# Optimization experiments

Measured on AMD Instinct MI355X. Metric: run time of the kernel, lower is better.

Reference implementation:

```python
import jax, jax.numpy as jnp
import numpy as np

S = 1
R = 64
INV_T = 100.0
EVAL_STEPS = 7  # module in eval mode
EPS = 1e-6


def setup_inputs() -> dict:
    key = jax.random.key(0)
    kx, kb = jax.random.split(key)
    B, C, H, W = 8, 512, 64, 64
    x = jax.random.uniform(kx, (B, C, H, W), dtype=jnp.float32)  # non-negative input for NMF
    bases = jax.random.uniform(kb, (B * S, C // S, R), dtype=jnp.float32)
    # F.normalize(bases, dim=1): L2-normalize along D
    bases = bases / jnp.linalg.norm(bases, axis=1, keepdims=True)
    return {"x": x, "bases": bases}


def reference(x, bases):
    B, C, H, W = x.shape
    D = C // S
    N = H * W
    xf = x.reshape(B * S, D, N)  # (BS, D, N)

    # initial coefficients: softmax(inv_t * x^T @ bases)
    coef = jax.nn.softmax(INV_T * jnp.einsum('bdn,bdr->bnr', xf, bases), axis=-1)

    def mu_step(carry, _):
        bases, coef = carry
        # update coef: coef *= (x^T bases) / (coef (bases^T bases) + eps)
        num = jnp.einsum('bdn,bdr->bnr', xf, bases)            # (BS, N, R)
        gram_b = jnp.einsum('bdr,bds->brs', bases, bases)      # (BS, R, R)
        coef = coef * num / (jnp.einsum('bnr,brs->bns', coef, gram_b) + EPS)
        # update bases: bases *= (x coef) / (bases (coef^T coef) + eps)
        num_b = jnp.einsum('bdn,bnr->bdr', xf, coef)           # (BS, D, R)
        gram_c = jnp.einsum('bnr,bns->brs', coef, coef)        # (BS, R, R)
        bases = bases * num_b / (jnp.einsum('bdr,brs->bds', bases, gram_c) + EPS)
        return (bases, coef), None

    (bases, coef), _ = jax.lax.scan(mu_step, (bases, coef), None, length=EVAL_STEPS)

    # compute_coef: one extra coef multiplicative update
    num = jnp.einsum('bdn,bdr->bnr', xf, bases)
    gram_b = jnp.einsum('bdr,bds->brs', bases, bases)
    coef = coef * num / (jnp.einsum('bnr,brs->bns', coef, gram_b) + EPS)

    out = jnp.einsum('bdr,bnr->bdn', bases, coef)  # bases @ coef^T
    return out.reshape(B, C, H, W)
```

## Files before the change

kernel.cpp:

```cpp
#include <hip/hip_runtime.h>
#include <math.h>

#define BATCH 8
#define DD 512
#define NN 4096
#define RR 64
#define NSTEPS 7
#define INV_T 100.0f
#define EPSV 1e-6f
#define GC_SCALE (1.0f / 1024.0f)
#define GC_UNSCALE 1024.0f

typedef __attribute__((ext_vector_type(8))) _Float16 f16x8;
typedef __attribute__((ext_vector_type(4))) _Float16 f16x4;
typedef __attribute__((ext_vector_type(4))) float f32x4;

__device__ __forceinline__ _Float16 f2h(float f) { return (_Float16)f; }

__device__ __forceinline__ void do_xcvt(const float* x, _Float16* x_h,
                                        _Float16* xT_h, int b, int d0, int n0,
                                        int tid, char* smem) {
  _Float16(*t)[72] = (_Float16(*)[72])smem;
  const size_t xbase = (size_t)(b * DD + d0) * NN + n0;
#pragma unroll
  for (int i = 0; i < 4; ++i) {
    const int idx = tid + i * 256;
    const int row = idx >> 4, c4 = (idx & 15) * 4;
    const float4 v = *(const float4*)(x + xbase + (size_t)row * NN + c4);
    f16x4 hv = {f2h(v.x), f2h(v.y), f2h(v.z), f2h(v.w)};
    *(f16x4*)(x_h + xbase + (size_t)row * NN + c4) = hv;
    *(f16x4*)&t[row][c4] = hv;
  }
  __syncthreads();
  const size_t tbase = (size_t)(b * NN + n0) * DD + d0;
#pragma unroll
  for (int i = 0; i < 4; ++i) {
    const int idx = tid + i * 256;
    const int row = idx >> 4, c4 = (idx & 15) * 4;
    f16x4 wv = {t[c4][row], t[c4 + 1][row], t[c4 + 2][row], t[c4 + 3][row]};
    *(f16x4*)(xT_h + tbase + (size_t)row * DD + c4) = wv;
  }
}

__device__ __forceinline__ void do_bases_prep(const float* bin, float* bases32,
                                              _Float16* bases_h,
                                              _Float16* basesT_h, int b, int d0,
                                              int tid, char* smem) {
  float(*t)[65] = (float(*)[65])smem;
  const size_t base = (size_t)(b * DD + d0) * RR;
#pragma unroll
  for (int i = 0; i < 4; ++i) {
    const int idx = tid + i * 256;
    const int row = idx >> 4, c4 = (idx & 15) * 4;
    const float4 v = *(const float4*)(bin + base + row * RR + c4);
    *(float4*)(bases32 + base + row * RR + c4) = v;
    f16x4 hv = {f2h(v.x), f2h(v.y), f2h(v.z), f2h(v.w)};
    *(f16x4*)(bases_h + base + row * RR + c4) = hv;
    t[row][c4] = v.x; t[row][c4 + 1] = v.y; t[row][c4 + 2] = v.z; t[row][c4 + 3] = v.w;
  }
  __syncthreads();
#pragma unroll
  for (int i = 0; i < 4; ++i) {
    const int idx = tid + i * 256;
    const int row = idx >> 4, c4 = (idx & 15) * 4;
    f16x4 wv = {f2h(t[c4][row]), f2h(t[c4 + 1][row]), f2h(t[c4 + 2][row]),
                f2h(t[c4 + 3][row])};
    *(f16x4*)(basesT_h + (size_t)(b * RR + row) * DD + d0 + c4) = wv;
  }
}

__device__ __forceinline__ void do_gramb_init(const _Float16* basesT_h,
                                              float* pgb, int b, int tid, int w,
                                              int lo, int hi) {
  const _Float16* ap = basesT_h + (size_t)(b * RR + w * 16 + lo) * DD + hi * 8;
  const _Float16* bp = basesT_h + (size_t)(b * RR + lo) * DD + hi * 8;
  f32x4 acc[4] = {};
#pragma unroll
  for (int ks = 0; ks < 16; ++ks) {
    f16x8 a = *(const f16x8*)(ap + ks * 32);
#pragma unroll
    for (int c = 0; c < 4; ++c) {
      f16x8 bb = *(const f16x8*)(bp + (size_t)c * 16 * DD + ks * 32);
      acc[c] = __builtin_amdgcn_mfma_f32_16x16x32_f16(a, bb, acc[c], 0, 0, 0);
    }
  }
  float* op = pgb + (size_t)(b * 8) * 4096;
#pragma unroll
  for (int c = 0; c < 4; ++c)
#pragma unroll
    for (int r = 0; r < 4; ++r)
      op[(w * 16 + hi * 4 + r) * RR + c * 16 + lo] = acc[c][r];
  for (int sp = 1; sp < 8; ++sp)
    for (int idx = tid; idx < 4096; idx += 256)
      pgb[(size_t)(b * 8 + sp) * 4096 + idx] = 0.f;
}

template <int MODE>
__device__ __forceinline__ void do_coef(const _Float16* xT_h,
                                        const _Float16* basesT_h,
                                        const float* pgb, _Float16* coefT_h,
                                        int b, int nt, int tid, int w, int lo,
                                        int hi, char* smem) {
  _Float16* gsm = (_Float16*)smem;
  _Float16(*ct)[72] = (_Float16(*)[72])(smem + 8192);
  const int n0 = nt * 64;
  if (MODE == 1) {
    for (int idx = tid; idx < 4096; idx += 256) {
      float s = 0.f;
#pragma unroll
      for (int sp = 0; sp < 8; ++sp)
        s += pgb[(size_t)(b * 8 + sp) * 4096 + idx];
      gsm[idx] = f2h(s);
    }
#pragma unroll
    for (int i = 0; i < 2; ++i) {
      const int idx = tid + i * 256;
      const int r = idx >> 3, n8 = (idx & 7) * 8;
      f16x8 vv = *(const f16x8*)(coefT_h + (size_t)(b * RR + r) * NN + n0 + n8);
#pragma unroll
      for (int j = 0; j < 8; ++j) ct[n8 + j][r] = vv[j];
    }
    __syncthreads();
  }

  const _Float16* ap = xT_h + (size_t)(b * NN + n0 + w * 16 + lo) * DD + hi * 8;
  const _Float16* bp = basesT_h + (size_t)(b * RR + lo) * DD + hi * 8;
  f32x4 acc[4] = {};
#pragma unroll
  for (int ks = 0; ks < 16; ++ks) {
    f16x8 a = *(const f16x8*)(ap + ks * 32);
#pragma unroll
    for (int c = 0; c < 4; ++c) {
      f16x8 bb = *(const f16x8*)(bp + (size_t)c * 16 * DD + ks * 32);
      acc[c] = __builtin_amdgcn_mfma_f32_16x16x32_f16(a, bb, acc[c], 0, 0, 0);
    }
  }

  float v[4][4];

  if (MODE == 0) {
#pragma unroll
    for (int reg = 0; reg < 4; ++reg) {
      float m = fmaxf(fmaxf(acc[0][reg], acc[1][reg]),
                      fmaxf(acc[2][reg], acc[3][reg]));
      m = fmaxf(m, __shfl_xor(m, 1));
      m = fmaxf(m, __shfl_xor(m, 2));
      m = fmaxf(m, __shfl_xor(m, 4));
      m = fmaxf(m, __shfl_xor(m, 8));
      float s = 0.f, e[4];
#pragma unroll
      for (int c = 0; c < 4; ++c) {
        e[c] = expf(INV_T * (acc[c][reg] - m));
        s += e[c];
      }
      s += __shfl_xor(s, 1);
      s += __shfl_xor(s, 2);
      s += __shfl_xor(s, 4);
      s += __shfl_xor(s, 8);
      const float inv = 1.f / s;
#pragma unroll
      for (int c = 0; c < 4; ++c) v[c][reg] = e[c] * inv;
    }
  } else {
    f32x4 den[4] = {};
#pragma unroll
    for (int kk = 0; kk < 2; ++kk) {
      f16x8 a = *(const f16x8*)&ct[w * 16 + lo][kk * 32 + hi * 8];
#pragma unroll
      for (int c = 0; c < 4; ++c) {
        f16x8 gv = *(const f16x8*)(gsm + (c * 16 + lo) * RR + kk * 32 + hi * 8);
        den[c] = __builtin_amdgcn_mfma_f32_16x16x32_f16(a, gv, den[c], 0, 0, 0);
      }
    }
#pragma unroll
    for (int reg = 0; reg < 4; ++reg)
#pragma unroll
      for (int c = 0; c < 4; ++c) {
        const float oldc = (float)ct[w * 16 + hi * 4 + reg][c * 16 + lo];
        v[c][reg] = oldc * acc[c][reg] / (den[c][reg] + EPSV);
      }
  }

#pragma unroll
  for (int c = 0; c < 4; ++c) {
    f16x4 t4 = {f2h(v[c][0]), f2h(v[c][1]), f2h(v[c][2]), f2h(v[c][3])};
    *(f16x4*)(coefT_h + (size_t)(b * RR + c * 16 + lo) * NN + n0 + w * 16 + hi * 4) = t4;
  }
}

__device__ __forceinline__ void do_numb(const _Float16* x_h,
                                        const _Float16* coefT_h, float* pnb,
                                        int kc, int dt, int b, int w, int lo,
                                        int hi) {
  const _Float16* ap =
      x_h + (size_t)(b * DD + dt * 64 + w * 16 + lo) * NN + kc * 1024 + hi * 8;
  const _Float16* bp = coefT_h + (size_t)(b * RR + lo) * NN + kc * 1024 + hi * 8;
  f32x4 acc[4] = {};
#pragma unroll 4
  for (int ks = 0; ks < 32; ++ks) {
    f16x8 a = *(const f16x8*)(ap + ks * 32);
#pragma unroll
    for (int c = 0; c < 4; ++c) {
      f16x8 bb = *(const f16x8*)(bp + (size_t)c * 16 * NN + ks * 32);
      acc[c] = __builtin_amdgcn_mfma_f32_16x16x32_f16(a, bb, acc[c], 0, 0, 0);
    }
  }
  float* op = pnb + ((size_t)((b * 4 + kc) * DD) + dt * 64 + w * 16 + hi * 4) * RR;
#pragma unroll
  for (int c = 0; c < 4; ++c)
#pragma unroll
    for (int r = 0; r < 4; ++r) op[r * RR + c * 16 + lo] = acc[c][r];
}

__device__ __forceinline__ void do_gramc(const _Float16* coefT_h, float* pgram,
                                         int sp, int b, int w, int lo, int hi) {
  const int k0 = sp * 256;
  const _Float16* ap = coefT_h + (size_t)(b * RR + w * 16 + lo) * NN + k0 + hi * 8;
  const _Float16* bp = coefT_h + (size_t)(b * RR + lo) * NN + k0 + hi * 8;
  f32x4 acc[4] = {};
#pragma unroll
  for (int ks = 0; ks < 8; ++ks) {
    f16x8 a = *(const f16x8*)(ap + ks * 32);
#pragma unroll
    for (int c = 0; c < 4; ++c) {
      f16x8 bb = *(const f16x8*)(bp + (size_t)c * 16 * NN + ks * 32);
      acc[c] = __builtin_amdgcn_mfma_f32_16x16x32_f16(a, bb, acc[c], 0, 0, 0);
    }
  }
  float* op = pgram + ((size_t)(b * 16 + sp) * RR + w * 16 + hi * 4) * RR;
#pragma unroll
  for (int c = 0; c < 4; ++c)
#pragma unroll
    for (int r = 0; r < 4; ++r) op[r * RR + c * 16 + lo] = acc[c][r];
}

__device__ __forceinline__ void do_bases_upd(const float* pnb,
                                             const float* pgram, float* bases32,
                                             _Float16* bases_h,
                                             _Float16* basesT_h, float* pgb,
                                             int dt, int b, int tid, int tx,
                                             int ty, char* smem) {
  float* bsm = (float*)smem;
  _Float16* gsh = (_Float16*)(smem + 16640);
  float* bg = bases32 + (size_t)(b * DD + dt * 64) * RR;
  for (int idx = tid; idx < 4096; idx += 256) {
    const int row = idx >> 6, cc = idx & 63;
    bsm[row * 65 + cc] = bg[row * 64 + cc];
  }
  for (int idx = tid; idx < 4096; idx += 256) {
    float s = 0.f;
#pragma unroll
    for (int sp = 0; sp < 16; ++sp)
      s += pgram[(size_t)(b * 16 + sp) * 4096 + idx];
    gsh[idx] = f2h(s * GC_SCALE);
  }
  __syncthreads();

  float nb[4][4];
#pragma unroll
  for (int i = 0; i < 4; ++i) {
    float4 s = make_float4(0.f, 0.f, 0.f, 0.f);
#pragma unroll
    for (int kc = 0; kc < 4; ++kc) {
      const float4 vv = *(const float4*)(pnb +
          (((size_t)b * 4 + kc) * DD + dt * 64 + ty * 4 + i) * RR + tx * 4);
      s.x += vv.x; s.y += vv.y; s.z += vv.z; s.w += vv.w;
    }
    nb[i][0] = s.x; nb[i][1] = s.y; nb[i][2] = s.z; nb[i][3] = s.w;
  }

  float den[4][4] = {};
  for (int s = 0; s < 64; ++s) {
    float a[4];
#pragma unroll
    for (int i = 0; i < 4; ++i) a[i] = bsm[(ty * 4 + i) * 65 + s];
    const f16x4 gv = *(const f16x4*)&gsh[s * 64 + tx * 4];
    const float g4[4] = {(float)gv[0], (float)gv[1], (float)gv[2], (float)gv[3]};
#pragma unroll
    for (int i = 0; i < 4; ++i)
#pragma unroll
      for (int j = 0; j < 4; ++j) den[i][j] = fmaf(a[i], g4[j], den[i][j]);
  }

  float v[4][4];
#pragma unroll
  for (int i = 0; i < 4; ++i) {
    float4 vv;
#pragma unroll
    for (int j = 0; j < 4; ++j) {
      const float oldb = bsm[(ty * 4 + i) * 65 + tx * 4 + j];
      v[i][j] = oldb * nb[i][j] / fmaf(den[i][j], GC_UNSCALE, EPSV);
    }
    vv.x = v[i][0]; vv.y = v[i][1]; vv.z = v[i][2]; vv.w = v[i][3];
    *(float4*)&bg[(ty * 4 + i) * 64 + tx * 4] = vv;
    f16x4 bv = {f2h(v[i][0]), f2h(v[i][1]), f2h(v[i][2]), f2h(v[i][3])};
    *(f16x4*)(bases_h + (size_t)(b * DD + dt * 64 + ty * 4 + i) * RR + tx * 4) = bv;
  }
#pragma unroll
  for (int j = 0; j < 4; ++j) {
    f16x4 tv = {f2h(v[0][j]), f2h(v[1][j]), f2h(v[2][j]), f2h(v[3][j])};
    *(f16x4*)(basesT_h + (size_t)(b * RR + tx * 4 + j) * DD + dt * 64 + ty * 4) = tv;
  }
  __syncthreads();
#pragma unroll
  for (int i = 0; i < 4; ++i)
#pragma unroll
    for (int j = 0; j < 4; ++j) bsm[(ty * 4 + i) * 65 + tx * 4 + j] = v[i][j];
  __syncthreads();

  float pa[4][4] = {};
  for (int d = 0; d < 64; ++d) {
    float a[4], bb[4];
#pragma unroll
    for (int i = 0; i < 4; ++i) a[i] = bsm[d * 65 + ty * 4 + i];
#pragma unroll
    for (int j = 0; j < 4; ++j) bb[j] = bsm[d * 65 + tx * 4 + j];
#pragma unroll
    for (int i = 0; i < 4; ++i)
#pragma unroll
      for (int j = 0; j < 4; ++j) pa[i][j] = fmaf(a[i], bb[j], pa[i][j]);
  }
  float* pp = pgb + (size_t)(b * 8 + dt) * 4096;
#pragma unroll
  for (int i = 0; i < 4; ++i) {
    float4 vv = make_float4(pa[i][0], pa[i][1], pa[i][2], pa[i][3]);
    *(float4*)(pp + (ty * 4 + i) * 64 + tx * 4) = vv;
  }
}

__device__ __forceinline__ void do_out(const _Float16* bases_h,
                                       const _Float16* coefT_h, float* out,
                                       int nt, int dt, int b, int tid, int w,
                                       int lo, int hi, char* smem) {
  _Float16(*ct)[72] = (_Float16(*)[72])smem;
  const int n0 = nt * 64;
#pragma unroll
  for (int i = 0; i < 2; ++i) {
    const int idx = tid + i * 256;
    const int r = idx >> 3, n8 = (idx & 7) * 8;
    f16x8 vv = *(const f16x8*)(coefT_h + (size_t)(b * RR + r) * NN + n0 + n8);
#pragma unroll
    for (int j = 0; j < 8; ++j) ct[n8 + j][r] = vv[j];
  }
  __syncthreads();
  const _Float16* ap =
      bases_h + (size_t)(b * DD + dt * 64 + w * 16 + lo) * RR + hi * 8;
  f32x4 acc[4] = {};
#pragma unroll
  for (int kk = 0; kk < 2; ++kk) {
    f16x8 a = *(const f16x8*)(ap + kk * 32);
#pragma unroll
    for (int c = 0; c < 4; ++c) {
      f16x8 bb = *(const f16x8*)&ct[c * 16 + lo][kk * 32 + hi * 8];
      acc[c] = __builtin_amdgcn_mfma_f32_16x16x32_f16(a, bb, acc[c], 0, 0, 0);
    }
  }
  float* op = out + (size_t)(b * DD + dt * 64 + w * 16 + hi * 4) * NN + n0;
#pragma unroll
  for (int c = 0; c < 4; ++c)
#pragma unroll
    for (int r = 0; r < 4; ++r) op[(size_t)r * NN + c * 16 + lo] = acc[c][r];
}

__global__ __launch_bounds__(256) void k_prep(const float* x, const float* bin,
                                              float* b32, _Float16* x_h,
                                              _Float16* xT_h, _Float16* bh,
                                              _Float16* bth) {
  __shared__ __attribute__((aligned(16))) char smem[16640];
  const int g = blockIdx.x, tid = threadIdx.x;
  if (g < 4096)
    do_xcvt(x, x_h, xT_h, g >> 9, ((g >> 6) & 7) * 64, (g & 63) * 64, tid, smem);
  else {
    const int q = g - 4096;
    do_bases_prep(bin, b32, bh, bth, q >> 3, (q & 7) * 64, tid, smem);
  }
}
__global__ __launch_bounds__(256) void k_init(const _Float16* xT_h,
                                              const _Float16* basesT_h,
                                              float* pgb, _Float16* coefT_h) {
  __shared__ __attribute__((aligned(16))) char smem[17408];
  const int tid = threadIdx.x, w = tid >> 6, l = tid & 63, lo = l & 15,
            hi = l >> 4;
  const int g = blockIdx.x;
  if (g < 512)
    do_coef<0>(xT_h, basesT_h, pgb, coefT_h, g >> 6, g & 63, tid, w, lo, hi,
               smem);
  else
    do_gramb_init(basesT_h, pgb, g - 512, tid, w, lo, hi);
}
__global__ __launch_bounds__(256) void k_coef1(const _Float16* xT_h,
                                               const _Float16* basesT_h,
                                               const float* pgb,
                                               _Float16* coefT_h) {
  __shared__ __attribute__((aligned(16))) char smem[17408];
  const int tid = threadIdx.x, w = tid >> 6, l = tid & 63, lo = l & 15,
            hi = l >> 4;
  do_coef<1>(xT_h, basesT_h, pgb, coefT_h, blockIdx.x >> 6, blockIdx.x & 63,
             tid, w, lo, hi, smem);
}
__global__ __launch_bounds__(256) void k_nbgc(const _Float16* x_h,
                                              const _Float16* coefT_h,
                                              float* pnb, float* pgram) {
  const int tid = threadIdx.x, w = tid >> 6, l = tid & 63, lo = l & 15,
            hi = l >> 4;
  const int g = blockIdx.x;
  if (g < 256)
    do_numb(x_h, coefT_h, pnb, g & 3, (g >> 2) & 7, g >> 5, w, lo, hi);
  else
    do_gramc(coefT_h, pgram, (g - 256) & 15, (g - 256) >> 4, w, lo, hi);
}
__global__ __launch_bounds__(256) void k_bupd(const float* pnb,
                                              const float* pgram, float* b32,
                                              _Float16* bh, _Float16* bth,
                                              float* pgb) {
  __shared__ __attribute__((aligned(16))) char smem[24832];
  do_bases_upd(pnb, pgram, b32, bh, bth, pgb, blockIdx.x & 7, blockIdx.x >> 3,
               threadIdx.x, threadIdx.x & 15, threadIdx.x >> 4, smem);
}
__global__ __launch_bounds__(256) void k_out(const _Float16* bh,
                                             const _Float16* ct, float* out) {
  __shared__ __attribute__((aligned(16))) char smem[9216];
  const int tid = threadIdx.x, w = tid >> 6, l = tid & 63, lo = l & 15,
            hi = l >> 4;
  do_out(bh, ct, out, blockIdx.x, blockIdx.y, blockIdx.z, tid, w, lo, hi, smem);
}

extern "C" void kernel_launch(void* const* d_in, const int* in_sizes, int n_in,
                              void* d_out, int out_size, void* d_ws,
                              size_t ws_size, hipStream_t stream) {
  (void)in_sizes; (void)n_in; (void)out_size; (void)ws_size;
  const float* x = (const float*)d_in[0];
  const float* bin = (const float*)d_in[1];
  float* W = (float*)d_ws;
  float* O = (float*)d_out;

  float* bases32 = W;
  float* pnb = bases32 + 262144;
  float* pgram = pnb + 1048576;
  float* pgb = pgram + 524288;
  _Float16* coefT_h = (_Float16*)(pgb + 262144);
  _Float16* bases_h = coefT_h + 2097152;
  _Float16* basesT_h = bases_h + 262144;
  _Float16* xT_h = (_Float16*)O;
  _Float16* x_h = xT_h + (size_t)BATCH * NN * DD;

  k_prep<<<4160, 256, 0, stream>>>(x, bin, bases32, x_h, xT_h, bases_h,
                                   basesT_h);
  k_init<<<520, 256, 0, stream>>>(xT_h, basesT_h, pgb, coefT_h);
  for (int s = 0; s < NSTEPS; ++s) {
    k_coef1<<<512, 256, 0, stream>>>(xT_h, basesT_h, pgb, coefT_h);
    k_nbgc<<<384, 256, 0, stream>>>(x_h, coefT_h, pnb, pgram);
    k_bupd<<<64, 256, 0, stream>>>(pnb, pgram, bases32, bases_h, basesT_h, pgb);
  }
  k_coef1<<<512, 256, 0, stream>>>(xT_h, basesT_h, pgb, coefT_h);
  k_out<<<dim3(64, 8, BATCH), 256, 0, stream>>>(bases_h, coefT_h, O);
}
```

Before: 559.1 us.

## Split coef and numb work into finer blocks and pre-reduce gram_b once per step

The coefficient update now uses 32-column tiles with each wave computing two of four 16-wide output groups, doubling the grid to 1024 blocks. The num_b K-split goes from 4 to 8 chunks, doubling its grid and the partial buffer the bases update sums. The 8-way partial reduction of the bases Gram matrix, previously repeated in every coef block, moves into a small k_gb kernel that writes an fp16 gram_b once per step. This aims to fill more CUs and remove redundant reduction work, at the cost of an extra launch per step, extra partial-sum traffic, and reloading the x tile once per column-group wave.

```diff
diff --git a/kernel.cpp b/kernel.cpp
--- a/kernel.cpp
+++ b/kernel.cpp
@@ -70,7 +70,7 @@
 }
 
 __device__ __forceinline__ void do_gramb_init(const _Float16* basesT_h,
-                                              float* pgb, int b, int tid, int w,
+                                              _Float16* gram_b_h, int b, int w,
                                               int lo, int hi) {
   const _Float16* ap = basesT_h + (size_t)(b * RR + w * 16 + lo) * DD + hi * 8;
   const _Float16* bp = basesT_h + (size_t)(b * RR + lo) * DD + hi * 8;
@@ -84,45 +84,19 @@
       acc[c] = __builtin_amdgcn_mfma_f32_16x16x32_f16(a, bb, acc[c], 0, 0, 0);
     }
   }
-  float* op = pgb + (size_t)(b * 8) * 4096;
+  _Float16* op = gram_b_h + (size_t)b * 4096;
 #pragma unroll
   for (int c = 0; c < 4; ++c)
 #pragma unroll
     for (int r = 0; r < 4; ++r)
-      op[(w * 16 + hi * 4 + r) * RR + c * 16 + lo] = acc[c][r];
-  for (int sp = 1; sp < 8; ++sp)
-    for (int idx = tid; idx < 4096; idx += 256)
-      pgb[(size_t)(b * 8 + sp) * 4096 + idx] = 0.f;
-}
-
-template <int MODE>
-__device__ __forceinline__ void do_coef(const _Float16* xT_h,
-                                        const _Float16* basesT_h,
-                                        const float* pgb, _Float16* coefT_h,
-                                        int b, int nt, int tid, int w, int lo,
-                                        int hi, char* smem) {
-  _Float16* gsm = (_Float16*)smem;
-  _Float16(*ct)[72] = (_Float16(*)[72])(smem + 8192);
+      op[(w * 16 + hi * 4 + r) * RR + c * 16 + lo] = f2h(acc[c][r]);
+}
+
+__device__ __forceinline__ void do_coef0(const _Float16* xT_h,
+                                         const _Float16* basesT_h,
+                                         _Float16* coefT_h, int b, int nt,
+                                         int w, int lo, int hi) {
   const int n0 = nt * 64;
-  if (MODE == 1) {
-    for (int idx = tid; idx < 4096; idx += 256) {
-      float s = 0.f;
-#pragma unroll
-      for (int sp = 0; sp < 8; ++sp)
-        s += pgb[(size_t)(b * 8 + sp) * 4096 + idx];
-      gsm[idx] = f2h(s);
-    }
-#pragma unroll
-    for (int i = 0; i < 2; ++i) {
-      const int idx = tid + i * 256;
-      const int r = idx >> 3, n8 = (idx & 7) * 8;
-      f16x8 vv = *(const f16x8*)(coefT_h + (size_t)(b * RR + r) * NN + n0 + n8);
-#pragma unroll
-      for (int j = 0; j < 8; ++j) ct[n8 + j][r] = vv[j];
-    }
-    __syncthreads();
-  }
-
   const _Float16* ap = xT_h + (size_t)(b * NN + n0 + w * 16 + lo) * DD + hi * 8;
   const _Float16* bp = basesT_h + (size_t)(b * RR + lo) * DD + hi * 8;
   f32x4 acc[4] = {};
@@ -135,56 +109,86 @@
       acc[c] = __builtin_amdgcn_mfma_f32_16x16x32_f16(a, bb, acc[c], 0, 0, 0);
     }
   }
-
   float v[4][4];
-
-  if (MODE == 0) {
-#pragma unroll
-    for (int reg = 0; reg < 4; ++reg) {
-      float m = fmaxf(fmaxf(acc[0][reg], acc[1][reg]),
-                      fmaxf(acc[2][reg], acc[3][reg]));
-      m = fmaxf(m, __shfl_xor(m, 1));
-      m = fmaxf(m, __shfl_xor(m, 2));
-      m = fmaxf(m, __shfl_xor(m, 4));
-      m = fmaxf(m, __shfl_xor(m, 8));
-      float s = 0.f, e[4];
-#pragma unroll
-      for (int c = 0; c < 4; ++c) {
-        e[c] = expf(INV_T * (acc[c][reg] - m));
-        s += e[c];
-      }
-      s += __shfl_xor(s, 1);
-      s += __shfl_xor(s, 2);
-      s += __shfl_xor(s, 4);
-      s += __shfl_xor(s, 8);
-      const float inv = 1.f / s;
-#pragma unroll
-      for (int c = 0; c < 4; ++c) v[c][reg] = e[c] * inv;
-    }
-  } else {
-    f32x4 den[4] = {};
-#pragma unroll
-    for (int kk = 0; kk < 2; ++kk) {
-      f16x8 a = *(const f16x8*)&ct[w * 16 + lo][kk * 32 + hi * 8];
-#pragma unroll
-      for (int c = 0; c < 4; ++c) {
-        f16x8 gv = *(const f16x8*)(gsm + (c * 16 + lo) * RR + kk * 32 + hi * 8);
-        den[c] = __builtin_amdgcn_mfma_f32_16x16x32_f16(a, gv, den[c], 0, 0, 0);
-      }
-    }
-#pragma unroll
-    for (int reg = 0; reg < 4; ++reg)
-#pragma unroll
-      for (int c = 0; c < 4; ++c) {
-        const float oldc = (float)ct[w * 16 + hi * 4 + reg][c * 16 + lo];
-        v[c][reg] = oldc * acc[c][reg] / (den[c][reg] + EPSV);
-      }
-  }
-
+#pragma unroll
+  for (int reg = 0; reg < 4; ++reg) {
+    float m = fmaxf(fmaxf(acc[0][reg], acc[1][reg]),
+                    fmaxf(acc[2][reg], acc[3][reg]));
+    m = fmaxf(m, __shfl_xor(m, 1));
+    m = fmaxf(m, __shfl_xor(m, 2));
+    m = fmaxf(m, __shfl_xor(m, 4));
+    m = fmaxf(m, __shfl_xor(m, 8));
+    float s = 0.f, e[4];
+#pragma unroll
+    for (int c = 0; c < 4; ++c) {
+      e[c] = expf(INV_T * (acc[c][reg] - m));
+      s += e[c];
+    }
+    s += __shfl_xor(s, 1);
+    s += __shfl_xor(s, 2);
+    s += __shfl_xor(s, 4);
+    s += __shfl_xor(s, 8);
+    const float inv = 1.f / s;
+#pragma unroll
+    for (int c = 0; c < 4; ++c) v[c][reg] = e[c] * inv;
+  }
 #pragma unroll
   for (int c = 0; c < 4; ++c) {
     f16x4 t4 = {f2h(v[c][0]), f2h(v[c][1]), f2h(v[c][2]), f2h(v[c][3])};
     *(f16x4*)(coefT_h + (size_t)(b * RR + c * 16 + lo) * NN + n0 + w * 16 + hi * 4) = t4;
+  }
+}
+
+__device__ __forceinline__ void do_coef_upd(const _Float16* xT_h,
+                                            const _Float16* basesT_h,
+                                            const _Float16* gram_b_h,
+                                            _Float16* coefT_h, int b, int n0,
+                                            int tid, int w, int lo, int hi,
+                                            char* smem) {
+  _Float16(*ct)[72] = (_Float16(*)[72])smem;
+  {
+    const int r = tid >> 2, n8 = (tid & 3) * 8;
+    f16x8 vv = *(const f16x8*)(coefT_h + (size_t)(b * RR + r) * NN + n0 + n8);
+#pragma unroll
+    for (int j = 0; j < 8; ++j) ct[n8 + j][r] = vv[j];
+  }
+  __syncthreads();
+  const int nb = (w >> 1) * 16;
+  const int cb = (w & 1) * 2;
+
+  const _Float16* ap = xT_h + (size_t)(b * NN + n0 + nb + lo) * DD + hi * 8;
+  const _Float16* bp = basesT_h + (size_t)(b * RR + cb * 16 + lo) * DD + hi * 8;
+  f32x4 acc[2] = {};
+#pragma unroll
+  for (int ks = 0; ks < 16; ++ks) {
+    f16x8 a = *(const f16x8*)(ap + ks * 32);
+#pragma unroll
+    for (int c = 0; c < 2; ++c) {
+      f16x8 bb = *(const f16x8*)(bp + (size_t)c * 16 * DD + ks * 32);
+      acc[c] = __builtin_amdgcn_mfma_f32_16x16x32_f16(a, bb, acc[c], 0, 0, 0);
+    }
+  }
+  f32x4 den[2] = {};
+#pragma unroll
+  for (int kk = 0; kk < 2; ++kk) {
+    f16x8 a = *(const f16x8*)&ct[nb + lo][kk * 32 + hi * 8];
+#pragma unroll
+    for (int c = 0; c < 2; ++c) {
+      f16x8 gv = *(const f16x8*)(gram_b_h + (size_t)b * 4096 +
+                                 ((cb + c) * 16 + lo) * RR + kk * 32 + hi * 8);
+      den[c] = __builtin_amdgcn_mfma_f32_16x16x32_f16(a, gv, den[c], 0, 0, 0);
+    }
+  }
+#pragma unroll
+  for (int c = 0; c < 2; ++c) {
+    f16x4 t4;
+#pragma unroll
+    for (int reg = 0; reg < 4; ++reg) {
+      const float oldc = (float)ct[nb + hi * 4 + reg][(cb + c) * 16 + lo];
+      t4[reg] = f2h(oldc * acc[c][reg] / (den[c][reg] + EPSV));
+    }
+    *(f16x4*)(coefT_h + (size_t)(b * RR + (cb + c) * 16 + lo) * NN + n0 + nb +
+              hi * 4) = t4;
   }
 }
 
@@ -193,11 +197,11 @@
                                         int kc, int dt, int b, int w, int lo,
                                         int hi) {
   const _Float16* ap =
-      x_h + (size_t)(b * DD + dt * 64 + w * 16 + lo) * NN + kc * 1024 + hi * 8;
-  const _Float16* bp = coefT_h + (size_t)(b * RR + lo) * NN + kc * 1024 + hi * 8;
+      x_h + (size_t)(b * DD + dt * 64 + w * 16 + lo) * NN + kc * 512 + hi * 8;
+  const _Float16* bp = coefT_h + (size_t)(b * RR + lo) * NN + kc * 512 + hi * 8;
   f32x4 acc[4] = {};
-#pragma unroll 4
-  for (int ks = 0; ks < 32; ++ks) {
+#pragma unroll
+  for (int ks = 0; ks < 16; ++ks) {
     f16x8 a = *(const f16x8*)(ap + ks * 32);
 #pragma unroll
     for (int c = 0; c < 4; ++c) {
@@ -205,7 +209,7 @@
       acc[c] = __builtin_amdgcn_mfma_f32_16x16x32_f16(a, bb, acc[c], 0, 0, 0);
     }
   }
-  float* op = pnb + ((size_t)((b * 4 + kc) * DD) + dt * 64 + w * 16 + hi * 4) * RR;
+  float* op = pnb + ((size_t)((b * 8 + kc) * DD) + dt * 64 + w * 16 + hi * 4) * RR;
 #pragma unroll
   for (int c = 0; c < 4; ++c)
 #pragma unroll
@@ -261,9 +265,9 @@
   for (int i = 0; i < 4; ++i) {
     float4 s = make_float4(0.f, 0.f, 0.f, 0.f);
 #pragma unroll
-    for (int kc = 0; kc < 4; ++kc) {
+    for (int kc = 0; kc < 8; ++kc) {
       const float4 vv = *(const float4*)(pnb +
-          (((size_t)b * 4 + kc) * DD + dt * 64 + ty * 4 + i) * RR + tx * 4);
+          (((size_t)b * 8 + kc) * DD + dt * 64 + ty * 4 + i) * RR + tx * 4);
       s.x += vv.x; s.y += vv.y; s.z += vv.z; s.w += vv.w;
     }
     nb[i][0] = s.x; nb[i][1] = s.y; nb[i][2] = s.z; nb[i][3] = s.w;
@@ -377,26 +381,25 @@
 }
 __global__ __launch_bounds__(256) void k_init(const _Float16* xT_h,
                                               const _Float16* basesT_h,
-                                              float* pgb, _Float16* coefT_h) {
-  __shared__ __attribute__((aligned(16))) char smem[17408];
+                                              _Float16* gram_b_h,
+                                              _Float16* coefT_h) {
   const int tid = threadIdx.x, w = tid >> 6, l = tid & 63, lo = l & 15,
             hi = l >> 4;
   const int g = blockIdx.x;
   if (g < 512)
-    do_coef<0>(xT_h, basesT_h, pgb, coefT_h, g >> 6, g & 63, tid, w, lo, hi,
-               smem);
+    do_coef0(xT_h, basesT_h, coefT_h, g >> 6, g & 63, w, lo, hi);
   else
-    do_gramb_init(basesT_h, pgb, g - 512, tid, w, lo, hi);
+    do_gramb_init(basesT_h, gram_b_h, g - 512, w, lo, hi);
 }
 __global__ __launch_bounds__(256) void k_coef1(const _Float16* xT_h,
                                                const _Float16* basesT_h,
-                                               const float* pgb,
+                                               const _Float16* gram_b_h,
                                                _Float16* coefT_h) {
-  __shared__ __attribute__((aligned(16))) char smem[17408];
+  __shared__ __attribute__((aligned(16))) char smem[4608];
   const int tid = threadIdx.x, w = tid >> 6, l = tid & 63, lo = l & 15,
             hi = l >> 4;
-  do_coef<1>(xT_h, basesT_h, pgb, coefT_h, blockIdx.x >> 6, blockIdx.x & 63,
-             tid, w, lo, hi, smem);
+  const int b = blockIdx.x >> 7, n0 = (blockIdx.x & 127) * 32;
+  do_coef_upd(xT_h, basesT_h, gram_b_h, coefT_h, b, n0, tid, w, lo, hi, smem);
 }
 __global__ __launch_bounds__(256) void k_nbgc(const _Float16* x_h,
                                               const _Float16* coefT_h,
@@ -404,10 +407,12 @@
   const int tid = threadIdx.x, w = tid >> 6, l = tid & 63, lo = l & 15,
             hi = l >> 4;
   const int g = blockIdx.x;
-  if (g < 256)
-    do_numb(x_h, coefT_h, pnb, g & 3, (g >> 2) & 7, g >> 5, w, lo, hi);
-  else
-    do_gramc(coefT_h, pgram, (g - 256) & 15, (g - 256) >> 4, w, lo, hi);
+  if (g < 512)
+    do_numb(x_h, coefT_h, pnb, g & 7, (g >> 3) & 7, g >> 6, w, lo, hi);
+  else {
+    const int q = g - 512;
+    do_gramc(coefT_h, pgram, q & 15, q >> 4, w, lo, hi);
+  }
 }
 __global__ __launch_bounds__(256) void k_bupd(const float* pnb,
                                               const float* pgram, float* b32,
@@ -416,6 +421,19 @@
   __shared__ __attribute__((aligned(16))) char smem[24832];
   do_bases_upd(pnb, pgram, b32, bh, bth, pgb, blockIdx.x & 7, blockIdx.x >> 3,
                threadIdx.x, threadIdx.x & 15, threadIdx.x >> 4, smem);
+}
+__global__ __launch_bounds__(256) void k_gb(const float* pgb,
+                                            _Float16* gram_b_h) {
+  const int b = blockIdx.x >> 3;
+  const int e0 = (blockIdx.x & 7) * 512 + threadIdx.x;
+#pragma unroll
+  for (int t = 0; t < 2; ++t) {
+    const int e = e0 + t * 256;
+    float s = 0.f;
+#pragma unroll
+    for (int sp = 0; sp < 8; ++sp) s += pgb[(size_t)(b * 8 + sp) * 4096 + e];
+    gram_b_h[(size_t)b * 4096 + e] = f2h(s);
+  }
 }
 __global__ __launch_bounds__(256) void k_out(const _Float16* bh,
                                              const _Float16* ct, float* out) {
@@ -436,22 +454,24 @@
 
   float* bases32 = W;
   float* pnb = bases32 + 262144;
-  float* pgram = pnb + 1048576;
+  float* pgram = pnb + 2097152;
   float* pgb = pgram + 524288;
   _Float16* coefT_h = (_Float16*)(pgb + 262144);
   _Float16* bases_h = coefT_h + 2097152;
   _Float16* basesT_h = bases_h + 262144;
+  _Float16* gram_b_h = basesT_h + 262144;
   _Float16* xT_h = (_Float16*)O;
   _Float16* x_h = xT_h + (size_t)BATCH * NN * DD;
 
   k_prep<<<4160, 256, 0, stream>>>(x, bin, bases32, x_h, xT_h, bases_h,
                                    basesT_h);
-  k_init<<<520, 256, 0, stream>>>(xT_h, basesT_h, pgb, coefT_h);
+  k_init<<<520, 256, 0, stream>>>(xT_h, basesT_h, gram_b_h, coefT_h);
   for (int s = 0; s < NSTEPS; ++s) {
-    k_coef1<<<512, 256, 0, stream>>>(xT_h, basesT_h, pgb, coefT_h);
-    k_nbgc<<<384, 256, 0, stream>>>(x_h, coefT_h, pnb, pgram);
+    k_coef1<<<1024, 256, 0, stream>>>(xT_h, basesT_h, gram_b_h, coefT_h);
+    k_nbgc<<<640, 256, 0, stream>>>(x_h, coefT_h, pnb, pgram);
     k_bupd<<<64, 256, 0, stream>>>(pnb, pgram, bases32, bases_h, basesT_h, pgb);
-  }
-  k_coef1<<<512, 256, 0, stream>>>(xT_h, basesT_h, pgb, coefT_h);
+    k_gb<<<64, 256, 0, stream>>>(pgb, gram_b_h);
+  }
+  k_coef1<<<1024, 256, 0, stream>>>(xT_h, basesT_h, gram_b_h, coefT_h);
   k_out<<<dim3(64, 8, BATCH), 256, 0, stream>>>(bases_h, coefT_h, O);
 }
```

After: 587.1 us. 1.05x slower.

## Fuse softmax init with first coef update and final coef update with output

Applied to the files above, without the earlier changes.

Adds a fused init kernel that computes the softmax coefficients and immediately applies the first multiplicative coef update, using an fp16 gram_b from a small separate kernel. Adds a fused final kernel that performs the last coef update and the bases @ coef^T output in one pass. It also moves the fp16 x copies into the workspace when it is large enough and hoists the shared-memory barrier after the main MFMA loop. Together these remove two kernel launches and the round trips of coefficients through global memory. The fallback path for a small workspace runs an extra coef update and reads x from the same buffer the output is written to, so it looks incorrect.

```diff
diff --git a/kernel.cpp b/kernel.cpp
--- a/kernel.cpp
+++ b/kernel.cpp
@@ -69,9 +69,10 @@
   }
 }
 
-__device__ __forceinline__ void do_gramb_init(const _Float16* basesT_h,
-                                              float* pgb, int b, int tid, int w,
-                                              int lo, int hi) {
+__global__ __launch_bounds__(256) void k_gb0(const _Float16* basesT_h,
+                                             _Float16* gram_b_h) {
+  const int b = blockIdx.x, tid = threadIdx.x;
+  const int w = tid >> 6, l = tid & 63, lo = l & 15, hi = l >> 4;
   const _Float16* ap = basesT_h + (size_t)(b * RR + w * 16 + lo) * DD + hi * 8;
   const _Float16* bp = basesT_h + (size_t)(b * RR + lo) * DD + hi * 8;
   f32x4 acc[4] = {};
@@ -84,43 +85,110 @@
       acc[c] = __builtin_amdgcn_mfma_f32_16x16x32_f16(a, bb, acc[c], 0, 0, 0);
     }
   }
-  float* op = pgb + (size_t)(b * 8) * 4096;
+  _Float16* op = gram_b_h + (size_t)b * 4096;
 #pragma unroll
   for (int c = 0; c < 4; ++c)
 #pragma unroll
     for (int r = 0; r < 4; ++r)
-      op[(w * 16 + hi * 4 + r) * RR + c * 16 + lo] = acc[c][r];
-  for (int sp = 1; sp < 8; ++sp)
-    for (int idx = tid; idx < 4096; idx += 256)
-      pgb[(size_t)(b * 8 + sp) * 4096 + idx] = 0.f;
-}
-
-template <int MODE>
-__device__ __forceinline__ void do_coef(const _Float16* xT_h,
-                                        const _Float16* basesT_h,
-                                        const float* pgb, _Float16* coefT_h,
-                                        int b, int nt, int tid, int w, int lo,
-                                        int hi, char* smem) {
+      op[(w * 16 + hi * 4 + r) * RR + c * 16 + lo] = f2h(acc[c][r]);
+}
+
+__global__ __launch_bounds__(256) void k_initf(const _Float16* xT_h,
+                                               const _Float16* basesT_h,
+                                               const _Float16* gram_b_h,
+                                               _Float16* coefT_h) {
+  __shared__ __attribute__((aligned(16))) _Float16 ct[64][72];
+  const int tid = threadIdx.x, w = tid >> 6, l = tid & 63, lo = l & 15,
+            hi = l >> 4;
+  const int b = blockIdx.x >> 6, n0 = (blockIdx.x & 63) * 64;
+
+  const _Float16* ap = xT_h + (size_t)(b * NN + n0 + w * 16 + lo) * DD + hi * 8;
+  const _Float16* bp = basesT_h + (size_t)(b * RR + lo) * DD + hi * 8;
+  f32x4 acc[4] = {};
+#pragma unroll
+  for (int ks = 0; ks < 16; ++ks) {
+    f16x8 a = *(const f16x8*)(ap + ks * 32);
+#pragma unroll
+    for (int c = 0; c < 4; ++c) {
+      f16x8 bb = *(const f16x8*)(bp + (size_t)c * 16 * DD + ks * 32);
+      acc[c] = __builtin_amdgcn_mfma_f32_16x16x32_f16(a, bb, acc[c], 0, 0, 0);
+    }
+  }
+  float v0[4][4];
+#pragma unroll
+  for (int reg = 0; reg < 4; ++reg) {
+    float m = fmaxf(fmaxf(acc[0][reg], acc[1][reg]),
+                    fmaxf(acc[2][reg], acc[3][reg]));
+    m = fmaxf(m, __shfl_xor(m, 1));
+    m = fmaxf(m, __shfl_xor(m, 2));
+    m = fmaxf(m, __shfl_xor(m, 4));
+    m = fmaxf(m, __shfl_xor(m, 8));
+    float s = 0.f, e[4];
+#pragma unroll
+    for (int c = 0; c < 4; ++c) {
+      e[c] = expf(INV_T * (acc[c][reg] - m));
+      s += e[c];
+    }
+    s += __shfl_xor(s, 1);
+    s += __shfl_xor(s, 2);
+    s += __shfl_xor(s, 4);
+    s += __shfl_xor(s, 8);
+    const float inv = 1.f / s;
+#pragma unroll
+    for (int c = 0; c < 4; ++c) v0[c][reg] = e[c] * inv;
+  }
+#pragma unroll
+  for (int reg = 0; reg < 4; ++reg)
+#pragma unroll
+    for (int c = 0; c < 4; ++c)
+      ct[w * 16 + hi * 4 + reg][c * 16 + lo] = f2h(v0[c][reg]);
+  __syncthreads();
+  f32x4 den[4] = {};
+#pragma unroll
+  for (int kk = 0; kk < 2; ++kk) {
+    f16x8 a = *(const f16x8*)&ct[w * 16 + lo][kk * 32 + hi * 8];
+#pragma unroll
+    for (int c = 0; c < 4; ++c) {
+      f16x8 gv = *(const f16x8*)(gram_b_h + (size_t)b * 4096 +
+                                 (c * 16 + lo) * RR + kk * 32 + hi * 8);
+      den[c] = __builtin_amdgcn_mfma_f32_16x16x32_f16(a, gv, den[c], 0, 0, 0);
+    }
+  }
+#pragma unroll
+  for (int c = 0; c < 4; ++c) {
+    f16x4 t4;
+#pragma unroll
+    for (int reg = 0; reg < 4; ++reg) {
+      const float oldc = (float)ct[w * 16 + hi * 4 + reg][c * 16 + lo];
+      t4[reg] = f2h(oldc * acc[c][reg] / (den[c][reg] + EPSV));
+    }
+    *(f16x4*)(coefT_h + (size_t)(b * RR + c * 16 + lo) * NN + n0 + w * 16 +
+              hi * 4) = t4;
+  }
+}
+
+__device__ __forceinline__ void do_coef1(const _Float16* xT_h,
+                                         const _Float16* basesT_h,
+                                         const float* pgb, _Float16* coefT_h,
+                                         int b, int nt, int tid, int w, int lo,
+                                         int hi, char* smem) {
   _Float16* gsm = (_Float16*)smem;
   _Float16(*ct)[72] = (_Float16(*)[72])(smem + 8192);
   const int n0 = nt * 64;
-  if (MODE == 1) {
-    for (int idx = tid; idx < 4096; idx += 256) {
-      float s = 0.f;
-#pragma unroll
-      for (int sp = 0; sp < 8; ++sp)
-        s += pgb[(size_t)(b * 8 + sp) * 4096 + idx];
-      gsm[idx] = f2h(s);
-    }
-#pragma unroll
-    for (int i = 0; i < 2; ++i) {
-      const int idx = tid + i * 256;
-      const int r = idx >> 3, n8 = (idx & 7) * 8;
-      f16x8 vv = *(const f16x8*)(coefT_h + (size_t)(b * RR + r) * NN + n0 + n8);
-#pragma unroll
-      for (int j = 0; j < 8; ++j) ct[n8 + j][r] = vv[j];
-    }
-    __syncthreads();
+  for (int idx = tid; idx < 4096; idx += 256) {
+    float s = 0.f;
+#pragma unroll
+    for (int sp = 0; sp < 8; ++sp)
+      s += pgb[(size_t)(b * 8 + sp) * 4096 + idx];
+    gsm[idx] = f2h(s);
+  }
+#pragma unroll
+  for (int i = 0; i < 2; ++i) {
+    const int idx = tid + i * 256;
+    const int r = idx >> 3, n8 = (idx & 7) * 8;
+    f16x8 vv = *(const f16x8*)(coefT_h + (size_t)(b * RR + r) * NN + n0 + n8);
+#pragma unroll
+    for (int j = 0; j < 8; ++j) ct[n8 + j][r] = vv[j];
   }
 
   const _Float16* ap = xT_h + (size_t)(b * NN + n0 + w * 16 + lo) * DD + hi * 8;
@@ -135,56 +203,27 @@
       acc[c] = __builtin_amdgcn_mfma_f32_16x16x32_f16(a, bb, acc[c], 0, 0, 0);
     }
   }
-
-  float v[4][4];
-
-  if (MODE == 0) {
+  __syncthreads();
+  f32x4 den[4] = {};
+#pragma unroll
+  for (int kk = 0; kk < 2; ++kk) {
+    f16x8 a = *(const f16x8*)&ct[w * 16 + lo][kk * 32 + hi * 8];
+#pragma unroll
+    for (int c = 0; c < 4; ++c) {
+      f16x8 gv = *(const f16x8*)(gsm + (c * 16 + lo) * RR + kk * 32 + hi * 8);
+      den[c] = __builtin_amdgcn_mfma_f32_16x16x32_f16(a, gv, den[c], 0, 0, 0);
+    }
+  }
+#pragma unroll
+  for (int c = 0; c < 4; ++c) {
+    f16x4 t4;
 #pragma unroll
     for (int reg = 0; reg < 4; ++reg) {
-      float m = fmaxf(fmaxf(acc[0][reg], acc[1][reg]),
-                      fmaxf(acc[2][reg], acc[3][reg]));
-      m = fmaxf(m, __shfl_xor(m, 1));
-      m = fmaxf(m, __shfl_xor(m, 2));
-      m = fmaxf(m, __shfl_xor(m, 4));
-      m = fmaxf(m, __shfl_xor(m, 8));
-      float s = 0.f, e[4];
-#pragma unroll
-      for (int c = 0; c < 4; ++c) {
-        e[c] = expf(INV_T * (acc[c][reg] - m));
-        s += e[c];
-      }
-      s += __shfl_xor(s, 1);
-      s += __shfl_xor(s, 2);
-      s += __shfl_xor(s, 4);
-      s += __shfl_xor(s, 8);
-      const float inv = 1.f / s;
-#pragma unroll
-      for (int c = 0; c < 4; ++c) v[c][reg] = e[c] * inv;
-    }
-  } else {
-    f32x4 den[4] = {};
-#pragma unroll
-    for (int kk = 0; kk < 2; ++kk) {
-      f16x8 a = *(const f16x8*)&ct[w * 16 + lo][kk * 32 + hi * 8];
-#pragma unroll
-      for (int c = 0; c < 4; ++c) {
-        f16x8 gv = *(const f16x8*)(gsm + (c * 16 + lo) * RR + kk * 32 + hi * 8);
-        den[c] = __builtin_amdgcn_mfma_f32_16x16x32_f16(a, gv, den[c], 0, 0, 0);
-      }
-    }
-#pragma unroll
-    for (int reg = 0; reg < 4; ++reg)
-#pragma unroll
-      for (int c = 0; c < 4; ++c) {
-        const float oldc = (float)ct[w * 16 + hi * 4 + reg][c * 16 + lo];
-        v[c][reg] = oldc * acc[c][reg] / (den[c][reg] + EPSV);
-      }
-  }
-
-#pragma unroll
-  for (int c = 0; c < 4; ++c) {
-    f16x4 t4 = {f2h(v[c][0]), f2h(v[c][1]), f2h(v[c][2]), f2h(v[c][3])};
-    *(f16x4*)(coefT_h + (size_t)(b * RR + c * 16 + lo) * NN + n0 + w * 16 + hi * 4) = t4;
+      const float oldc = (float)ct[w * 16 + hi * 4 + reg][c * 16 + lo];
+      t4[reg] = f2h(oldc * acc[c][reg] / (den[c][reg] + EPSV));
+    }
+    *(f16x4*)(coefT_h + (size_t)(b * RR + c * 16 + lo) * NN + n0 + w * 16 +
+              hi * 4) = t4;
   }
 }
 
@@ -328,12 +367,26 @@
   }
 }
 
-__device__ __forceinline__ void do_out(const _Float16* bases_h,
-                                       const _Float16* coefT_h, float* out,
-                                       int nt, int dt, int b, int tid, int w,
-                                       int lo, int hi, char* smem) {
-  _Float16(*ct)[72] = (_Float16(*)[72])smem;
-  const int n0 = nt * 64;
+__global__ __launch_bounds__(256) void k_cout(const _Float16* xT_h,
+                                              const _Float16* basesT_h,
+                                              const float* pgb,
+                                              const _Float16* coefT_h,
+                                              const _Float16* bases_h,
+                                              float* out) {
+  __shared__ __attribute__((aligned(16))) char smem[17408];
+  _Float16* gsm = (_Float16*)smem;
+  _Float16(*ct)[72] = (_Float16(*)[72])(smem + 8192);
+  const int tid = threadIdx.x, w = tid >> 6, l = tid & 63, lo = l & 15,
+            hi = l >> 4;
+  const int b = blockIdx.x >> 6, n0 = (blockIdx.x & 63) * 64;
+
+  for (int idx = tid; idx < 4096; idx += 256) {
+    float s = 0.f;
+#pragma unroll
+    for (int sp = 0; sp < 8; ++sp)
+      s += pgb[(size_t)(b * 8 + sp) * 4096 + idx];
+    gsm[idx] = f2h(s);
+  }
 #pragma unroll
   for (int i = 0; i < 2; ++i) {
     const int idx = tid + i * 256;
@@ -342,24 +395,65 @@
 #pragma unroll
     for (int j = 0; j < 8; ++j) ct[n8 + j][r] = vv[j];
   }
-  __syncthreads();
-  const _Float16* ap =
-      bases_h + (size_t)(b * DD + dt * 64 + w * 16 + lo) * RR + hi * 8;
+
+  const _Float16* ap = xT_h + (size_t)(b * NN + n0 + w * 16 + lo) * DD + hi * 8;
+  const _Float16* bp = basesT_h + (size_t)(b * RR + lo) * DD + hi * 8;
   f32x4 acc[4] = {};
 #pragma unroll
+  for (int ks = 0; ks < 16; ++ks) {
+    f16x8 a = *(const f16x8*)(ap + ks * 32);
+#pragma unroll
+    for (int c = 0; c < 4; ++c) {
+      f16x8 bb = *(const f16x8*)(bp + (size_t)c * 16 * DD + ks * 32);
+      acc[c] = __builtin_amdgcn_mfma_f32_16x16x32_f16(a, bb, acc[c], 0, 0, 0);
+    }
+  }
+  __syncthreads();
+  f32x4 den[4] = {};
+#pragma unroll
   for (int kk = 0; kk < 2; ++kk) {
-    f16x8 a = *(const f16x8*)(ap + kk * 32);
-#pragma unroll
-    for (int c = 0; c < 4; ++c) {
-      f16x8 bb = *(const f16x8*)&ct[c * 16 + lo][kk * 32 + hi * 8];
-      acc[c] = __builtin_amdgcn_mfma_f32_16x16x32_f16(a, bb, acc[c], 0, 0, 0);
-    }
-  }
-  float* op = out + (size_t)(b * DD + dt * 64 + w * 16 + hi * 4) * NN + n0;
+    f16x8 a = *(const f16x8*)&ct[w * 16 + lo][kk * 32 + hi * 8];
+#pragma unroll
+    for (int c = 0; c < 4; ++c) {
+      f16x8 gv = *(const f16x8*)(gsm + (c * 16 + lo) * RR + kk * 32 + hi * 8);
+      den[c] = __builtin_amdgcn_mfma_f32_16x16x32_f16(a, gv, den[c], 0, 0, 0);
+    }
+  }
+  float v[4][4];
 #pragma unroll
   for (int c = 0; c < 4; ++c)
 #pragma unroll
-    for (int r = 0; r < 4; ++r) op[(size_t)r * NN + c * 16 + lo] = acc[c][r];
+    for (int reg = 0; reg < 4; ++reg) {
+      const float oldc = (float)ct[w * 16 + hi * 4 + reg][c * 16 + lo];
+      v[c][reg] = oldc * acc[c][reg] / (den[c][reg] + EPSV);
+    }
+  __syncthreads();
+#pragma unroll
+  for (int c = 0; c < 4; ++c)
+#pragma unroll
+    for (int reg = 0; reg < 4; ++reg)
+      ct[w * 16 + hi * 4 + reg][c * 16 + lo] = f2h(v[c][reg]);
+  __syncthreads();
+
+  for (int dt = 0; dt < 8; ++dt) {
+    const _Float16* bap =
+        bases_h + (size_t)(b * DD + dt * 64 + w * 16 + lo) * RR + hi * 8;
+    f32x4 oacc[4] = {};
+#pragma unroll
+    for (int kk = 0; kk < 2; ++kk) {
+      f16x8 a = *(const f16x8*)(bap + kk * 32);
+#pragma unroll
+      for (int c = 0; c < 4; ++c) {
+        f16x8 bb = *(const f16x8*)&ct[c * 16 + lo][kk * 32 + hi * 8];
+        oacc[c] = __builtin_amdgcn_mfma_f32_16x16x32_f16(a, bb, oacc[c], 0, 0, 0);
+      }
+    }
+    float* op = out + (size_t)(b * DD + dt * 64 + w * 16 + hi * 4) * NN + n0;
+#pragma unroll
+    for (int c = 0; c < 4; ++c)
+#pragma unroll
+      for (int r = 0; r < 4; ++r) op[(size_t)r * NN + c * 16 + lo] = oacc[c][r];
+  }
 }
 
 __global__ __launch_bounds__(256) void k_prep(const float* x, const float* bin,
@@ -375,19 +469,6 @@
     do_bases_prep(bin, b32, bh, bth, q >> 3, (q & 7) * 64, tid, smem);
   }
 }
-__global__ __launch_bounds__(256) void k_init(const _Float16* xT_h,
-                                              const _Float16* basesT_h,
-                                              float* pgb, _Float16* coefT_h) {
-  __shared__ __attribute__((aligned(16))) char smem[17408];
-  const int tid = threadIdx.x, w = tid >> 6, l = tid & 63, lo = l & 15,
-            hi = l >> 4;
-  const int g = blockIdx.x;
-  if (g < 512)
-    do_coef<0>(xT_h, basesT_h, pgb, coefT_h, g >> 6, g & 63, tid, w, lo, hi,
-               smem);
-  else
-    do_gramb_init(basesT_h, pgb, g - 512, tid, w, lo, hi);
-}
 __global__ __launch_bounds__(256) void k_coef1(const _Float16* xT_h,
                                                const _Float16* basesT_h,
                                                const float* pgb,
@@ -395,8 +476,8 @@
   __shared__ __attribute__((aligned(16))) char smem[17408];
   const int tid = threadIdx.x, w = tid >> 6, l = tid & 63, lo = l & 15,
             hi = l >> 4;
-  do_coef<1>(xT_h, basesT_h, pgb, coefT_h, blockIdx.x >> 6, blockIdx.x & 63,
-             tid, w, lo, hi, smem);
+  do_coef1(xT_h, basesT_h, pgb, coefT_h, blockIdx.x >> 6, blockIdx.x & 63, tid,
+           w, lo, hi, smem);
 }
 __global__ __launch_bounds__(256) void k_nbgc(const _Float16* x_h,
                                               const _Float16* coefT_h,
@@ -406,8 +487,10 @@
   const int g = blockIdx.x;
   if (g < 256)
     do_numb(x_h, coefT_h, pnb, g & 3, (g >> 2) & 7, g >> 5, w, lo, hi);
-  else
-    do_gramc(coefT_h, pgram, (g - 256) & 15, (g - 256) >> 4, w, lo, hi);
+  else {
+    const int q = g - 256;
+    do_gramc(coefT_h, pgram, q & 15, q >> 4, w, lo, hi);
+  }
 }
 __global__ __launch_bounds__(256) void k_bupd(const float* pnb,
                                               const float* pgram, float* b32,
@@ -417,18 +500,11 @@
   do_bases_upd(pnb, pgram, b32, bh, bth, pgb, blockIdx.x & 7, blockIdx.x >> 3,
                threadIdx.x, threadIdx.x & 15, threadIdx.x >> 4, smem);
 }
-__global__ __launch_bounds__(256) void k_out(const _Float16* bh,
-                                             const _Float16* ct, float* out) {
-  __shared__ __attribute__((aligned(16))) char smem[9216];
-  const int tid = threadIdx.x, w = tid >> 6, l = tid & 63, lo = l & 15,
-            hi = l >> 4;
-  do_out(bh, ct, out, blockIdx.x, blockIdx.y, blockIdx.z, tid, w, lo, hi, smem);
-}
 
 extern "C" void kernel_launch(void* const* d_in, const int* in_sizes, int n_in,
                               void* d_out, int out_size, void* d_ws,
                               size_t ws_size, hipStream_t stream) {
-  (void)in_sizes; (void)n_in; (void)out_size; (void)ws_size;
+  (void)in_sizes; (void)n_in; (void)out_size;
   const float* x = (const float*)d_in[0];
   const float* bin = (const float*)d_in[1];
   float* W = (float*)d_ws;
@@ -441,17 +517,36 @@
   _Float16* coefT_h = (_Float16*)(pgb + 262144);
   _Float16* bases_h = coefT_h + 2097152;
   _Float16* basesT_h = bases_h + 262144;
-  _Float16* xT_h = (_Float16*)O;
-  _Float16* x_h = xT_h + (size_t)BATCH * NN * DD;
+  _Float16* gram_b_h = basesT_h + 262144;
+  _Float16* ws_end = gram_b_h + 32768;
+
+  const size_t xhalves = (size_t)BATCH * NN * DD;
+  const size_t need = ((char*)(ws_end + 2 * xhalves)) - (char*)W;
+  _Float16* xT_h;
+  _Float16* x_h;
+  const bool ws_fits = (ws_size >= need);
+  if (ws_fits) {
+    xT_h = ws_end;
+    x_h = xT_h + xhalves;
+  } else {
+    xT_h = (_Float16*)O;
+    x_h = xT_h + xhalves;
+  }
 
   k_prep<<<4160, 256, 0, stream>>>(x, bin, bases32, x_h, xT_h, bases_h,
                                    basesT_h);
-  k_init<<<520, 256, 0, stream>>>(xT_h, basesT_h, pgb, coefT_h);
+  k_gb0<<<BATCH, 256, 0, stream>>>(basesT_h, gram_b_h);
+  k_initf<<<512, 256, 0, stream>>>(xT_h, basesT_h, gram_b_h, coefT_h);
   for (int s = 0; s < NSTEPS; ++s) {
-    k_coef1<<<512, 256, 0, stream>>>(xT_h, basesT_h, pgb, coefT_h);
     k_nbgc<<<384, 256, 0, stream>>>(x_h, coefT_h, pnb, pgram);
     k_bupd<<<64, 256, 0, stream>>>(pnb, pgram, bases32, bases_h, basesT_h, pgb);
-  }
-  k_coef1<<<512, 256, 0, stream>>>(xT_h, basesT_h, pgb, coefT_h);
-  k_out<<<dim3(64, 8, BATCH), 256, 0, stream>>>(bases_h, coefT_h, O);
-}
+    if (s < NSTEPS - 1)
+      k_coef1<<<512, 256, 0, stream>>>(xT_h, basesT_h, pgb, coefT_h);
+  }
+  if (ws_fits) {
+    k_cout<<<512, 256, 0, stream>>>(xT_h, basesT_h, pgb, coefT_h, bases_h, O);
+  } else {
+    k_coef1<<<512, 256, 0, stream>>>(xT_h, basesT_h, pgb, coefT_h);
+    k_cout<<<512, 256, 0, stream>>>(xT_h, basesT_h, pgb, coefT_h, bases_h, O);
+  }
+}
```

New measurement: 520.2 us. -7.0%, faster.
